# Optimization experiments

Hardware: AMD Instinct MI355X
Metric: run time of the kernel (lower is better)

Reference implementation:

```python
import jax, jax.numpy as jnp
import numpy as np
from jax import lax

HIDDEN = 128

def setup_inputs() -> dict:
    key = jax.random.key(0)
    ks = jax.random.split(key, 8)
    B, S, V, D = 256, 512, 50000, 300
    x = jax.random.randint(ks[0], (B, S), 0, V, dtype=jnp.int64)
    emb = jax.random.normal(ks[1], (V, D), dtype=jnp.float32)
    s_ih = 1.0 / np.sqrt(HIDDEN)
    W_ih = jax.random.normal(ks[2], (HIDDEN, D), dtype=jnp.float32) * s_ih
    W_hh = jax.random.normal(ks[3], (HIDDEN, HIDDEN), dtype=jnp.float32) * s_ih
    b_ih = jax.random.normal(ks[4], (HIDDEN,), dtype=jnp.float32) * s_ih
    b_hh = jax.random.normal(ks[5], (HIDDEN,), dtype=jnp.float32) * s_ih
    fc_w = jax.random.normal(ks[6], (1, 2 * HIDDEN), dtype=jnp.float32) * (1.0 / np.sqrt(2 * HIDDEN))
    fc_b = jax.random.normal(ks[7], (1,), dtype=jnp.float32) * 0.01
    return {"x": x, "emb": emb, "W_ih": W_ih, "W_hh": W_hh,
            "b_ih": b_ih, "b_hh": b_hh, "fc_w": fc_w, "fc_b": fc_b}

def reference(x, emb, W_ih, W_hh, b_ih, b_hh, fc_w, fc_b):
    # Embedding lookup: [B,S] -> [B,S,D]
    xe = emb[x]
    # Precompute input projection for all timesteps: [B,S,H]
    xp = jnp.einsum('bsd,hd->bsh', xe, W_ih) + b_ih
    B = xp.shape[0]
    h0 = jnp.zeros((B, HIDDEN), dtype=xp.dtype)

    def step(h, xt):  # xt: [B,H]
        h = jnp.tanh(xt + h @ W_hh.T + b_hh)
        return h, h

    _, outs = lax.scan(step, h0, xp.transpose(1, 0, 2))  # outs: [S,B,H]
    outs = outs.transpose(1, 0, 2)  # [B,S,H]
    pooled = jnp.concatenate([outs.max(axis=1), outs.mean(axis=1)], axis=-1)  # [B,2H]
    return pooled @ fc_w.T + fc_b  # [B,1]
```

## Files before the change

kernel.cpp:

```cpp
#include <hip/hip_runtime.h>

#define HID    128
#define SEQ    512
#define BATCH  256
#define DIM    300
#define VOCAB  50000
#define WT_FLOATS 40960

__global__ __launch_bounds__(256)
void wtrans_kernel(const float* __restrict__ Wih, float* __restrict__ Wt)
{
    int idx = blockIdx.x * 256 + threadIdx.x;
    if (idx < HID * DIM) {
        int h = idx / DIM;
        int k = idx - h * DIM;
        Wt[(k >> 2) * (HID * 4) + h * 4 + (k & 3)] = Wih[idx];
    }
}

#define ETP 20
#define VT  16
__global__ __launch_bounds__(256)
void proj_fast256(const float* __restrict__ emb,
                  const float* __restrict__ Wt,
                  const float* __restrict__ bih,
                  const float* __restrict__ bhh,
                  float* __restrict__ P)
{
    __shared__ float et[DIM][ETP];
    const int t   = threadIdx.x;
    const int hp  = t & 63;
    const int rg4 = ((t >> 6) & 3) * 4;
    const int v0  = blockIdx.x * VT;

    {
        const int rr = t >> 4;
        const int kk = t & 15;
        const float* src = emb + (size_t)(v0 + rr) * DIM;
        #pragma unroll
        for (int p = 0; p < 5; ++p) {
            const int f4 = kk + 16 * p;
            if (f4 < DIM / 4) {
                const float4 ev = *(const float4*)(src + f4 * 4);
                et[4 * f4 + 0][rr] = ev.x;
                et[4 * f4 + 1][rr] = ev.y;
                et[4 * f4 + 2][rr] = ev.z;
                et[4 * f4 + 3][rr] = ev.w;
            }
        }
    }
    __syncthreads();

    float a00=0.f,a10=0.f,a20=0.f,a30=0.f;
    float a01=0.f,a11=0.f,a21=0.f,a31=0.f;

    const float* wp0 = Wt + hp * 4;
    const float* wp1 = Wt + (hp + 64) * 4;

    for (int k4 = 0; k4 < DIM / 4; ++k4) {
        const float4 wa4 = *(const float4*)(wp0 + k4 * (HID * 4));
        const float4 wb4 = *(const float4*)(wp1 + k4 * (HID * 4));
        #pragma unroll
        for (int jj = 0; jj < 4; ++jj) {
            const float wa = (jj==0)?wa4.x:(jj==1)?wa4.y:(jj==2)?wa4.z:wa4.w;
            const float wb = (jj==0)?wb4.x:(jj==1)?wb4.y:(jj==2)?wb4.z:wb4.w;
            const int k = k4 * 4 + jj;
            const float4 e0 = *(const float4*)(&et[k][rg4]);
            a00 = fmaf(wa, e0.x, a00);  a01 = fmaf(wb, e0.x, a01);
            a10 = fmaf(wa, e0.y, a10);  a11 = fmaf(wb, e0.y, a11);
            a20 = fmaf(wa, e0.z, a20);  a21 = fmaf(wb, e0.z, a21);
            a30 = fmaf(wa, e0.w, a30);  a31 = fmaf(wb, e0.w, a31);
        }
    }

    const float bb0 = bih[hp] + bhh[hp];
    const float bb1 = bih[hp + 64] + bhh[hp + 64];
    float* dst = P + (size_t)(v0 + rg4) * HID;
    dst[0*HID + hp] = a00 + bb0;  dst[0*HID + hp + 64] = a01 + bb1;
    dst[1*HID + hp] = a10 + bb0;  dst[1*HID + hp + 64] = a11 + bb1;
    dst[2*HID + hp] = a20 + bb0;  dst[2*HID + hp + 64] = a21 + bb1;
    dst[3*HID + hp] = a30 + bb0;  dst[3*HID + hp + 64] = a31 + bb1;
}

__global__ __launch_bounds__(128)
void proj_fallback(const float* __restrict__ emb,
                   const float* __restrict__ Wih,
                   const float* __restrict__ bih,
                   const float* __restrict__ bhh,
                   float* __restrict__ P)
{
    __shared__ float et[DIM][ETP];
    const int t  = threadIdx.x;
    const int hp = t & 63;
    const int rg8 = (t >> 6) * 8;
    const int v0 = blockIdx.x * VT;

    #pragma unroll
    for (int r = 0; r < VT; ++r) {
        const float* src = emb + (size_t)(v0 + r) * DIM;
        for (int k = t; k < DIM; k += 128)
            et[k][r] = src[k];
    }
    __syncthreads();

    float a00=0.f,a10=0.f,a20=0.f,a30=0.f,a40=0.f,a50=0.f,a60=0.f,a70=0.f;
    float a01=0.f,a11=0.f,a21=0.f,a31=0.f,a41=0.f,a51=0.f,a61=0.f,a71=0.f;

    const float* w0 = Wih + (size_t)hp * DIM;
    const float* w1 = Wih + (size_t)(hp + 64) * DIM;

    for (int k4 = 0; k4 < DIM / 4; ++k4) {
        const float4 wa4 = *(const float4*)(w0 + k4 * 4);
        const float4 wb4 = *(const float4*)(w1 + k4 * 4);
        #pragma unroll
        for (int jj = 0; jj < 4; ++jj) {
            const float wa = (jj==0)?wa4.x:(jj==1)?wa4.y:(jj==2)?wa4.z:wa4.w;
            const float wb = (jj==0)?wb4.x:(jj==1)?wb4.y:(jj==2)?wb4.z:wb4.w;
            const int k = k4 * 4 + jj;
            const float4 e0 = *(const float4*)(&et[k][rg8]);
            const float4 e1 = *(const float4*)(&et[k][rg8 + 4]);
            a00 = fmaf(wa, e0.x, a00);  a01 = fmaf(wb, e0.x, a01);
            a10 = fmaf(wa, e0.y, a10);  a11 = fmaf(wb, e0.y, a11);
            a20 = fmaf(wa, e0.z, a20);  a21 = fmaf(wb, e0.z, a21);
            a30 = fmaf(wa, e0.w, a30);  a31 = fmaf(wb, e0.w, a31);
            a40 = fmaf(wa, e1.x, a40);  a41 = fmaf(wb, e1.x, a41);
            a50 = fmaf(wa, e1.y, a50);  a51 = fmaf(wb, e1.y, a51);
            a60 = fmaf(wa, e1.z, a60);  a61 = fmaf(wb, e1.z, a61);
            a70 = fmaf(wa, e1.w, a70);  a71 = fmaf(wb, e1.w, a71);
        }
    }

    const float bb0 = bih[hp] + bhh[hp];
    const float bb1 = bih[hp + 64] + bhh[hp + 64];
    float* dst = P + (size_t)(v0 + rg8) * HID;
    dst[0*HID + hp] = a00 + bb0;  dst[0*HID + hp + 64] = a01 + bb1;
    dst[1*HID + hp] = a10 + bb0;  dst[1*HID + hp + 64] = a11 + bb1;
    dst[2*HID + hp] = a20 + bb0;  dst[2*HID + hp + 64] = a21 + bb1;
    dst[3*HID + hp] = a30 + bb0;  dst[3*HID + hp + 64] = a31 + bb1;
    dst[4*HID + hp] = a40 + bb0;  dst[4*HID + hp + 64] = a41 + bb1;
    dst[5*HID + hp] = a50 + bb0;  dst[5*HID + hp + 64] = a51 + bb1;
    dst[6*HID + hp] = a60 + bb0;  dst[6*HID + hp + 64] = a61 + bb1;
    dst[7*HID + hp] = a70 + bb0;  dst[7*HID + hp + 64] = a71 + bb1;
}

__device__ __forceinline__ float quad_sum(float v)
{
    int x1 = __builtin_amdgcn_update_dpp(0, __float_as_int(v), 0xB1, 0xF, 0xF, true);
    v += __int_as_float(x1);
    int x2 = __builtin_amdgcn_update_dpp(0, __float_as_int(v), 0x4E, 0xF, 0xF, true);
    v += __int_as_float(x2);
    return v;
}

__global__ __launch_bounds__(512)
void rnn_kernel(const int* __restrict__ x,
                const float* __restrict__ Whh,
                const float* __restrict__ P,
                const float* __restrict__ fcw,
                const float* __restrict__ fcb,
                float* __restrict__ out)
{
    __shared__ float h0b[HID];
    __shared__ float h1b[HID];
    __shared__ int   toff[SEQ];
    __shared__ float xb[2 * 64 * HID];
    __shared__ float red[HID];

    const int t  = threadIdx.x;
    const int b  = blockIdx.x;
    const int i  = t >> 2;
    const int kq = t & 3;

    toff[t] = x[b * SEQ + t] * HID;
    if (t < HID) h0b[t] = 0.f;

    float4 w[8];
    #pragma unroll
    for (int j = 0; j < 8; ++j) {
        const int pj = (j + 2 * kq) & 7;
        w[j] = *(const float4*)(Whh + (size_t)i * HID + kq * 32 + pj * 4);
    }
    __syncthreads();

#define STAGE(cn) do {                                                        \
        const int w_ = t >> 6, l_ = t & 63;                                   \
        const int base_ = ((cn) & 1) * (64 * HID);                            \
        _Pragma("unroll")                                                     \
        for (int q_ = 0; q_ < 4; ++q_) {                                      \
            const int row_ = w_ * 8 + q_ * 2 + (l_ >> 5);                     \
            const int col_ = (l_ & 31) * 4;                                   \
            const int off_ = toff[(cn) * 64 + row_] + col_;                   \
            const float4 v_ = *(const float4*)(P + off_);                     \
            *(float4*)(&xb[base_ + row_ * HID + col_]) = v_;                  \
        }                                                                     \
    } while (0)

    STAGE(0);
    __syncthreads();

    float hmax = -3.0e38f, hsum = 0.f;

#define STEP(HRD, HWR, XPTR, SOFF) do {                                       \
        const float xt = (XPTR)[(SOFF) * HID];                                \
        float ac0=0.f,ac1=0.f,ac2=0.f,ac3=0.f,ac4=0.f,ac5=0.f,ac6=0.f,ac7=0.f;\
        _Pragma("unroll")                                                     \
        for (int j = 0; j < 8; ++j) {                                         \
            const int pj = (j + 2 * kq) & 7;                                  \
            const float4 h4 = *(const float4*)((HRD) + kq * 32 + pj * 4);     \
            float* ap = (j==0)?&ac0:(j==1)?&ac1:(j==2)?&ac2:(j==3)?&ac3       \
                       :(j==4)?&ac4:(j==5)?&ac5:(j==6)?&ac6:&ac7;             \
            *ap = fmaf(w[j].x, h4.x, *ap);                                    \
            *ap = fmaf(w[j].y, h4.y, *ap);                                    \
            *ap = fmaf(w[j].z, h4.z, *ap);                                    \
            *ap = fmaf(w[j].w, h4.w, *ap);                                    \
        }                                                                     \
        float acc = ((ac0+ac1)+(ac2+ac3)) + ((ac4+ac5)+(ac6+ac7));            \
        acc = quad_sum(acc);                                                  \
        const float z = xt + acc;                                             \
        const float e = __builtin_amdgcn_exp2f(z * 2.8853900817779268f);      \
        const float hnew = fmaf(-2.f, __builtin_amdgcn_rcpf(e + 1.f), 1.f);   \
        hmax = fmaxf(hmax, hnew);                                             \
        hsum += hnew;                                                         \
        (HWR)[i] = hnew;                                                      \
        __syncthreads();                                                      \
    } while (0)

    for (int c = 0; c < 8; ++c) {
        if (c < 7) STAGE(c + 1);
        const float* xp = &xb[(c & 1) * (64 * HID) + i];
        #pragma unroll 4
        for (int u = 0; u < 32; ++u) {
            STEP(h0b, h1b, xp, u * 2);
            STEP(h1b, h0b, xp, u * 2 + 1);
        }
    }
#undef STEP
#undef STAGE

    if (kq == 0)
        red[i] = fcw[i] * hmax + fcw[HID + i] * (hsum * (1.f / 512.f));
    __syncthreads();
    if (t < 64) {
        float v = red[t] + red[t + 64];
        #pragma unroll
        for (int m = 32; m >= 1; m >>= 1) v += __shfl_xor(v, m);
        if (t == 0) out[b] = v + fcb[0];
    }
}

extern "C" void kernel_launch(void* const* d_in, const int* in_sizes, int n_in,
                              void* d_out, int out_size, void* d_ws, size_t ws_size,
                              hipStream_t stream)
{
    const int*   x   = (const int*)  d_in[0];
    const float* emb = (const float*)d_in[1];
    const float* Wih = (const float*)d_in[2];
    const float* Whh = (const float*)d_in[3];
    const float* bih = (const float*)d_in[4];
    const float* bhh = (const float*)d_in[5];
    const float* fcw = (const float*)d_in[6];
    const float* fcb = (const float*)d_in[7];

    float* base = (float*)d_ws;
    const size_t need = (WT_FLOATS + (size_t)VOCAB * HID) * sizeof(float);
    float* P;

    if (ws_size >= need) {
        float* Wt = base;
        P = base + WT_FLOATS;
        wtrans_kernel<<<(HID * DIM + 255) / 256, 256, 0, stream>>>(Wih, Wt);
        proj_fast256<<<VOCAB / VT, 256, 0, stream>>>(emb, Wt, bih, bhh, P);
    } else {
        P = base;
        proj_fallback<<<VOCAB / VT, 128, 0, stream>>>(emb, Wih, bih, bhh, P);
    }

    rnn_kernel<<<BATCH, 512, 0, stream>>>(x, Whh, P, fcw, fcb, (float*)d_out);
}
```

Measured before the change: 227.1 us.

## Share hidden-state loads across lanes with DPP broadcasts in the RNN recurrence

```diff
diff --git a/kernel.cpp b/kernel.cpp
--- a/kernel.cpp
+++ b/kernel.cpp
@@ -143,14 +143,7 @@
     dst[7*HID + hp] = a70 + bb0;  dst[7*HID + hp + 64] = a71 + bb1;
 }
 
-__device__ __forceinline__ float quad_sum(float v)
-{
-    int x1 = __builtin_amdgcn_update_dpp(0, __float_as_int(v), 0xB1, 0xF, 0xF, true);
-    v += __int_as_float(x1);
-    int x2 = __builtin_amdgcn_update_dpp(0, __float_as_int(v), 0x4E, 0xF, 0xF, true);
-    v += __int_as_float(x2);
-    return v;
-}
+#define HPAD 140
 
 __global__ __launch_bounds__(512)
 void rnn_kernel(const int* __restrict__ x,
@@ -160,25 +153,29 @@
                 const float* __restrict__ fcb,
                 float* __restrict__ out)
 {
-    __shared__ float h0b[HID];
-    __shared__ float h1b[HID];
+    __shared__ float h0b[HPAD];
+    __shared__ float h1b[HPAD];
     __shared__ int   toff[SEQ];
     __shared__ float xb[2 * 64 * HID];
     __shared__ float red[HID];
 
-    const int t  = threadIdx.x;
-    const int b  = blockIdx.x;
-    const int i  = t >> 2;
-    const int kq = t & 3;
+    const int t = threadIdx.x;
+    const int b = blockIdx.x;
+    const int i = ((t >> 4) << 2) | (t & 3);
+    const int c = (t >> 2) & 3;
+    const int j = t & 3;
+
+    const int roff = 36 * c + 8 * j;
+    const int hoff = i + ((i >> 5) << 2);
 
     toff[t] = x[b * SEQ + t] * HID;
-    if (t < HID) h0b[t] = 0.f;
-
-    float4 w[8];
+    if (t < HID) h0b[t + ((t >> 5) << 2)] = 0.f;
+
+    float4 w4[8];
     #pragma unroll
-    for (int j = 0; j < 8; ++j) {
-        const int pj = (j + 2 * kq) & 7;
-        w[j] = *(const float4*)(Whh + (size_t)i * HID + kq * 32 + pj * 4);
+    for (int k = 0; k < 4; ++k) {
+        w4[2*k]   = *(const float4*)(Whh + (size_t)i * HID + 32*c + 8*k);
+        w4[2*k+1] = *(const float4*)(Whh + (size_t)i * HID + 32*c + 8*k + 4);
     }
     __syncthreads();
 
@@ -200,45 +197,58 @@
 
     float hmax = -3.0e38f, hsum = 0.f;
 
+#define QB(V, CTRL) __int_as_float(__builtin_amdgcn_update_dpp(               \
+                        0, __float_as_int(V), (CTRL), 0xF, 0xF, true))
+
+#define KSTEP(ACC, EA, EB, KW0, KW1, CTRL) do {                               \
+        ACC = fmaf(KW0.x, QB(EA.x, CTRL), ACC);                               \
+        ACC = fmaf(KW0.y, QB(EA.y, CTRL), ACC);                               \
+        ACC = fmaf(KW0.z, QB(EA.z, CTRL), ACC);                               \
+        ACC = fmaf(KW0.w, QB(EA.w, CTRL), ACC);                               \
+        ACC = fmaf(KW1.x, QB(EB.x, CTRL), ACC);                               \
+        ACC = fmaf(KW1.y, QB(EB.y, CTRL), ACC);                               \
+        ACC = fmaf(KW1.z, QB(EB.z, CTRL), ACC);                               \
+        ACC = fmaf(KW1.w, QB(EB.w, CTRL), ACC);                               \
+    } while (0)
+
 #define STEP(HRD, HWR, XPTR, SOFF) do {                                       \
         const float xt = (XPTR)[(SOFF) * HID];                                \
-        float ac0=0.f,ac1=0.f,ac2=0.f,ac3=0.f,ac4=0.f,ac5=0.f,ac6=0.f,ac7=0.f;\
-        _Pragma("unroll")                                                     \
-        for (int j = 0; j < 8; ++j) {                                         \
-            const int pj = (j + 2 * kq) & 7;                                  \
-            const float4 h4 = *(const float4*)((HRD) + kq * 32 + pj * 4);     \
-            float* ap = (j==0)?&ac0:(j==1)?&ac1:(j==2)?&ac2:(j==3)?&ac3       \
-                       :(j==4)?&ac4:(j==5)?&ac5:(j==6)?&ac6:&ac7;             \
-            *ap = fmaf(w[j].x, h4.x, *ap);                                    \
-            *ap = fmaf(w[j].y, h4.y, *ap);                                    \
-            *ap = fmaf(w[j].z, h4.z, *ap);                                    \
-            *ap = fmaf(w[j].w, h4.w, *ap);                                    \
-        }                                                                     \
-        float acc = ((ac0+ac1)+(ac2+ac3)) + ((ac4+ac5)+(ac6+ac7));            \
-        acc = quad_sum(acc);                                                  \
-        const float z = xt + acc;                                             \
+        const float4 ea = *(const float4*)((HRD) + roff);                     \
+        const float4 eb = *(const float4*)((HRD) + roff + 4);                 \
+        float ac0 = 0.f, ac1 = 0.f, ac2 = 0.f, ac3 = 0.f;                     \
+        KSTEP(ac0, ea, eb, w4[0], w4[1], 0x00);                               \
+        KSTEP(ac1, ea, eb, w4[2], w4[3], 0x55);                               \
+        KSTEP(ac2, ea, eb, w4[4], w4[5], 0xAA);                               \
+        KSTEP(ac3, ea, eb, w4[6], w4[7], 0xFF);                               \
+        float s = (ac0 + ac1) + (ac2 + ac3);                                  \
+        s += __int_as_float(__builtin_amdgcn_update_dpp(                      \
+                 0, __float_as_int(s), 0x128, 0xF, 0xF, true));    \
+        s += __int_as_float(__builtin_amdgcn_update_dpp(                      \
+                 0, __float_as_int(s), 0x124, 0xF, 0xF, true));    \
+        const float z = xt + s;                                               \
         const float e = __builtin_amdgcn_exp2f(z * 2.8853900817779268f);      \
         const float hnew = fmaf(-2.f, __builtin_amdgcn_rcpf(e + 1.f), 1.f);   \
         hmax = fmaxf(hmax, hnew);                                             \
         hsum += hnew;                                                         \
-        (HWR)[i] = hnew;                                                      \
+        (HWR)[hoff] = hnew;     \
         __syncthreads();                                                      \
     } while (0)
 
-    for (int c = 0; c < 8; ++c) {
-        if (c < 7) STAGE(c + 1);
-        const float* xp = &xb[(c & 1) * (64 * HID) + i];
-        #pragma unroll 4
+    for (int cch = 0; cch < 8; ++cch) {
+        if (cch < 7) STAGE(cch + 1);
+        const float* xp = &xb[(cch & 1) * (64 * HID) + i];
+        #pragma unroll 2
         for (int u = 0; u < 32; ++u) {
             STEP(h0b, h1b, xp, u * 2);
             STEP(h1b, h0b, xp, u * 2 + 1);
         }
     }
 #undef STEP
+#undef KSTEP
+#undef QB
 #undef STAGE
 
-    if (kq == 0)
-        red[i] = fcw[i] * hmax + fcw[HID + i] * (hsum * (1.f / 512.f));
+    red[i] = fcw[i] * hmax + fcw[HID + i] * (hsum * (1.f / 512.f));
     __syncthreads();
     if (t < 64) {
         float v = red[t] + red[t + 64];
```

Measured after the change: 256.4 us. 12.9% more time.

## Compute vocabulary projection with bf16 MFMA instead of FP32 FMAs

Applied to the files above, without the earlier changes.

```diff
diff --git a/kernel.cpp b/kernel.cpp
--- a/kernel.cpp
+++ b/kernel.cpp
@@ -5,142 +5,125 @@
 #define BATCH  256
 #define DIM    300
 #define VOCAB  50000
-#define WT_FLOATS 40960
-
-__global__ __launch_bounds__(256)
-void wtrans_kernel(const float* __restrict__ Wih, float* __restrict__ Wt)
-{
-    int idx = blockIdx.x * 256 + threadIdx.x;
-    if (idx < HID * DIM) {
-        int h = idx / DIM;
-        int k = idx - h * DIM;
-        Wt[(k >> 2) * (HID * 4) + h * 4 + (k & 3)] = Wih[idx];
-    }
-}
-
-#define ETP 20
-#define VT  16
-__global__ __launch_bounds__(256)
-void proj_fast256(const float* __restrict__ emb,
-                  const float* __restrict__ Wt,
-                  const float* __restrict__ bih,
-                  const float* __restrict__ bhh,
-                  float* __restrict__ P)
-{
-    __shared__ float et[DIM][ETP];
-    const int t   = threadIdx.x;
-    const int hp  = t & 63;
-    const int rg4 = ((t >> 6) & 3) * 4;
-    const int v0  = blockIdx.x * VT;
-
-    {
-        const int rr = t >> 4;
-        const int kk = t & 15;
-        const float* src = emb + (size_t)(v0 + rr) * DIM;
+
+typedef short bf16x8 __attribute__((ext_vector_type(8)));
+typedef float f32x4  __attribute__((ext_vector_type(4)));
+
+#define KP   320
+#define LST  328
+
+__device__ __forceinline__ unsigned bf16_rtne(float v)
+{
+    unsigned u = __float_as_uint(v);
+    return (u + 0x7FFFu + ((u >> 16) & 1u)) >> 16;
+}
+
+__global__ __launch_bounds__(512)
+void proj_mfma(const float* __restrict__ emb,
+               const float* __restrict__ Wih,
+               const float* __restrict__ bih,
+               const float* __restrict__ bhh,
+               float* __restrict__ P)
+{
+    __shared__ unsigned short At[64 * LST];
+    __shared__ unsigned short Bt[128 * LST];
+
+    const int t  = threadIdx.x;
+    const int v0 = blockIdx.x * 64;
+
+    for (int c = t; c < 64 * 40; c += 512) {
+        const int row = c / 40;
+        const int ch  = c - row * 40;
+        int grow = v0 + row; if (grow > VOCAB - 1) grow = VOCAB - 1;
+        const float* src = emb + (size_t)grow * DIM;
+        const int k0 = ch * 8;
+        unsigned p0, p1, p2, p3;
+        if (k0 + 8 <= DIM) {
+            const float4 a = *(const float4*)(src + k0);
+            const float4 b = *(const float4*)(src + k0 + 4);
+            p0 = bf16_rtne(a.x) | (bf16_rtne(a.y) << 16);
+            p1 = bf16_rtne(a.z) | (bf16_rtne(a.w) << 16);
+            p2 = bf16_rtne(b.x) | (bf16_rtne(b.y) << 16);
+            p3 = bf16_rtne(b.z) | (bf16_rtne(b.w) << 16);
+        } else {
+            unsigned q[8];
+            #pragma unroll
+            for (int e = 0; e < 8; ++e) {
+                const int k = k0 + e;
+                q[e] = (k < DIM) ? bf16_rtne(src[k]) : 0u;
+            }
+            p0 = q[0] | (q[1] << 16);  p1 = q[2] | (q[3] << 16);
+            p2 = q[4] | (q[5] << 16);  p3 = q[6] | (q[7] << 16);
+        }
+        uint4 o = {p0, p1, p2, p3};
+        *(uint4*)(&At[row * LST + k0]) = o;
+    }
+
+    for (int c = t; c < 128 * 40; c += 512) {
+        const int row = c / 40;
+        const int ch  = c - row * 40;
+        const float* src = Wih + (size_t)row * DIM;
+        const int k0 = ch * 8;
+        unsigned p0, p1, p2, p3;
+        if (k0 + 8 <= DIM) {
+            const float4 a = *(const float4*)(src + k0);
+            const float4 b = *(const float4*)(src + k0 + 4);
+            p0 = bf16_rtne(a.x) | (bf16_rtne(a.y) << 16);
+            p1 = bf16_rtne(a.z) | (bf16_rtne(a.w) << 16);
+            p2 = bf16_rtne(b.x) | (bf16_rtne(b.y) << 16);
+            p3 = bf16_rtne(b.z) | (bf16_rtne(b.w) << 16);
+        } else {
+            unsigned q[8];
+            #pragma unroll
+            for (int e = 0; e < 8; ++e) {
+                const int k = k0 + e;
+                q[e] = (k < DIM) ? bf16_rtne(src[k]) : 0u;
+            }
+            p0 = q[0] | (q[1] << 16);  p1 = q[2] | (q[3] << 16);
+            p2 = q[4] | (q[5] << 16);  p3 = q[6] | (q[7] << 16);
+        }
+        uint4 o = {p0, p1, p2, p3};
+        *(uint4*)(&Bt[row * LST + k0]) = o;
+    }
+    __syncthreads();
+
+    const int lane = t & 63;
+    const int w    = t >> 6;
+    const int mt   = w >> 1;
+    const int nh   = w & 1;
+    const int lm   = lane & 15;
+    const int kg   = lane >> 4;
+
+    f32x4 acc0 = {0.f,0.f,0.f,0.f}, acc1 = {0.f,0.f,0.f,0.f};
+    f32x4 acc2 = {0.f,0.f,0.f,0.f}, acc3 = {0.f,0.f,0.f,0.f};
+
+    const unsigned short* arow = &At[(mt * 16 + lm) * LST + kg * 8];
+    const unsigned short* brow = &Bt[(nh * 64 + lm) * LST + kg * 8];
+
+    for (int k0 = 0; k0 < KP; k0 += 32) {
+        const bf16x8 af = *(const bf16x8*)(arow + k0);
+        const bf16x8 b0 = *(const bf16x8*)(brow + k0);
+        const bf16x8 b1 = *(const bf16x8*)(brow + 16 * LST + k0);
+        const bf16x8 b2 = *(const bf16x8*)(brow + 32 * LST + k0);
+        const bf16x8 b3 = *(const bf16x8*)(brow + 48 * LST + k0);
+        acc0 = __builtin_amdgcn_mfma_f32_16x16x32_bf16(af, b0, acc0, 0, 0, 0);
+        acc1 = __builtin_amdgcn_mfma_f32_16x16x32_bf16(af, b1, acc1, 0, 0, 0);
+        acc2 = __builtin_amdgcn_mfma_f32_16x16x32_bf16(af, b2, acc2, 0, 0, 0);
+        acc3 = __builtin_amdgcn_mfma_f32_16x16x32_bf16(af, b3, acc3, 0, 0, 0);
+    }
+
+    const int rbase = v0 + mt * 16 + kg * 4;
+    #pragma unroll
+    for (int nt = 0; nt < 4; ++nt) {
+        const int h = nh * 64 + nt * 16 + lm;
+        const float bb = bih[h] + bhh[h];
+        const f32x4 a = (nt == 0) ? acc0 : (nt == 1) ? acc1 : (nt == 2) ? acc2 : acc3;
         #pragma unroll
-        for (int p = 0; p < 5; ++p) {
-            const int f4 = kk + 16 * p;
-            if (f4 < DIM / 4) {
-                const float4 ev = *(const float4*)(src + f4 * 4);
-                et[4 * f4 + 0][rr] = ev.x;
-                et[4 * f4 + 1][rr] = ev.y;
-                et[4 * f4 + 2][rr] = ev.z;
-                et[4 * f4 + 3][rr] = ev.w;
-            }
-        }
-    }
-    __syncthreads();
-
-    float a00=0.f,a10=0.f,a20=0.f,a30=0.f;
-    float a01=0.f,a11=0.f,a21=0.f,a31=0.f;
-
-    const float* wp0 = Wt + hp * 4;
-    const float* wp1 = Wt + (hp + 64) * 4;
-
-    for (int k4 = 0; k4 < DIM / 4; ++k4) {
-        const float4 wa4 = *(const float4*)(wp0 + k4 * (HID * 4));
-        const float4 wb4 = *(const float4*)(wp1 + k4 * (HID * 4));
-        #pragma unroll
-        for (int jj = 0; jj < 4; ++jj) {
-            const float wa = (jj==0)?wa4.x:(jj==1)?wa4.y:(jj==2)?wa4.z:wa4.w;
-            const float wb = (jj==0)?wb4.x:(jj==1)?wb4.y:(jj==2)?wb4.z:wb4.w;
-            const int k = k4 * 4 + jj;
-            const float4 e0 = *(const float4*)(&et[k][rg4]);
-            a00 = fmaf(wa, e0.x, a00);  a01 = fmaf(wb, e0.x, a01);
-            a10 = fmaf(wa, e0.y, a10);  a11 = fmaf(wb, e0.y, a11);
-            a20 = fmaf(wa, e0.z, a20);  a21 = fmaf(wb, e0.z, a21);
-            a30 = fmaf(wa, e0.w, a30);  a31 = fmaf(wb, e0.w, a31);
-        }
-    }
-
-    const float bb0 = bih[hp] + bhh[hp];
-    const float bb1 = bih[hp + 64] + bhh[hp + 64];
-    float* dst = P + (size_t)(v0 + rg4) * HID;
-    dst[0*HID + hp] = a00 + bb0;  dst[0*HID + hp + 64] = a01 + bb1;
-    dst[1*HID + hp] = a10 + bb0;  dst[1*HID + hp + 64] = a11 + bb1;
-    dst[2*HID + hp] = a20 + bb0;  dst[2*HID + hp + 64] = a21 + bb1;
-    dst[3*HID + hp] = a30 + bb0;  dst[3*HID + hp + 64] = a31 + bb1;
-}
-
-__global__ __launch_bounds__(128)
-void proj_fallback(const float* __restrict__ emb,
-                   const float* __restrict__ Wih,
-                   const float* __restrict__ bih,
-                   const float* __restrict__ bhh,
-                   float* __restrict__ P)
-{
-    __shared__ float et[DIM][ETP];
-    const int t  = threadIdx.x;
-    const int hp = t & 63;
-    const int rg8 = (t >> 6) * 8;
-    const int v0 = blockIdx.x * VT;
-
-    #pragma unroll
-    for (int r = 0; r < VT; ++r) {
-        const float* src = emb + (size_t)(v0 + r) * DIM;
-        for (int k = t; k < DIM; k += 128)
-            et[k][r] = src[k];
-    }
-    __syncthreads();
-
-    float a00=0.f,a10=0.f,a20=0.f,a30=0.f,a40=0.f,a50=0.f,a60=0.f,a70=0.f;
-    float a01=0.f,a11=0.f,a21=0.f,a31=0.f,a41=0.f,a51=0.f,a61=0.f,a71=0.f;
-
-    const float* w0 = Wih + (size_t)hp * DIM;
-    const float* w1 = Wih + (size_t)(hp + 64) * DIM;
-
-    for (int k4 = 0; k4 < DIM / 4; ++k4) {
-        const float4 wa4 = *(const float4*)(w0 + k4 * 4);
-        const float4 wb4 = *(const float4*)(w1 + k4 * 4);
-        #pragma unroll
-        for (int jj = 0; jj < 4; ++jj) {
-            const float wa = (jj==0)?wa4.x:(jj==1)?wa4.y:(jj==2)?wa4.z:wa4.w;
-            const float wb = (jj==0)?wb4.x:(jj==1)?wb4.y:(jj==2)?wb4.z:wb4.w;
-            const int k = k4 * 4 + jj;
-            const float4 e0 = *(const float4*)(&et[k][rg8]);
-            const float4 e1 = *(const float4*)(&et[k][rg8 + 4]);
-            a00 = fmaf(wa, e0.x, a00);  a01 = fmaf(wb, e0.x, a01);
-            a10 = fmaf(wa, e0.y, a10);  a11 = fmaf(wb, e0.y, a11);
-            a20 = fmaf(wa, e0.z, a20);  a21 = fmaf(wb, e0.z, a21);
-            a30 = fmaf(wa, e0.w, a30);  a31 = fmaf(wb, e0.w, a31);
-            a40 = fmaf(wa, e1.x, a40);  a41 = fmaf(wb, e1.x, a41);
-            a50 = fmaf(wa, e1.y, a50);  a51 = fmaf(wb, e1.y, a51);
-            a60 = fmaf(wa, e1.z, a60);  a61 = fmaf(wb, e1.z, a61);
-            a70 = fmaf(wa, e1.w, a70);  a71 = fmaf(wb, e1.w, a71);
-        }
-    }
-
-    const float bb0 = bih[hp] + bhh[hp];
-    const float bb1 = bih[hp + 64] + bhh[hp + 64];
-    float* dst = P + (size_t)(v0 + rg8) * HID;
-    dst[0*HID + hp] = a00 + bb0;  dst[0*HID + hp + 64] = a01 + bb1;
-    dst[1*HID + hp] = a10 + bb0;  dst[1*HID + hp + 64] = a11 + bb1;
-    dst[2*HID + hp] = a20 + bb0;  dst[2*HID + hp + 64] = a21 + bb1;
-    dst[3*HID + hp] = a30 + bb0;  dst[3*HID + hp + 64] = a31 + bb1;
-    dst[4*HID + hp] = a40 + bb0;  dst[4*HID + hp + 64] = a41 + bb1;
-    dst[5*HID + hp] = a50 + bb0;  dst[5*HID + hp + 64] = a51 + bb1;
-    dst[6*HID + hp] = a60 + bb0;  dst[6*HID + hp + 64] = a61 + bb1;
-    dst[7*HID + hp] = a70 + bb0;  dst[7*HID + hp + 64] = a71 + bb1;
+        for (int r = 0; r < 4; ++r) {
+            const int row = rbase + r;
+            if (row < VOCAB) P[(size_t)row * HID + h] = a[r] + bb;
+        }
+    }
 }
 
 __device__ __forceinline__ float quad_sum(float v)
@@ -261,19 +244,8 @@
     const float* fcw = (const float*)d_in[6];
     const float* fcb = (const float*)d_in[7];
 
-    float* base = (float*)d_ws;
-    const size_t need = (WT_FLOATS + (size_t)VOCAB * HID) * sizeof(float);
-    float* P;
-
-    if (ws_size >= need) {
-        float* Wt = base;
-        P = base + WT_FLOATS;
-        wtrans_kernel<<<(HID * DIM + 255) / 256, 256, 0, stream>>>(Wih, Wt);
-        proj_fast256<<<VOCAB / VT, 256, 0, stream>>>(emb, Wt, bih, bhh, P);
-    } else {
-        P = base;
-        proj_fallback<<<VOCAB / VT, 128, 0, stream>>>(emb, Wih, bih, bhh, P);
-    }
-
+    float* P = (float*)d_ws;
+
+    proj_mfma<<<(VOCAB + 63) / 64, 512, 0, stream>>>(emb, Wih, bih, bhh, P);
     rnn_kernel<<<BATCH, 512, 0, stream>>>(x, Whh, P, fcw, fcb, (float*)d_out);
 }
```

Measured after the change: 228.1 us. No clear change (+0.4%).
